# Optimization experiments

Hardware: AMD Instinct MI355X
Metric: run time of the kernel (lower is better)

Reference implementation:

```python
import jax, jax.numpy as jnp
import numpy as np

B, SEQ, D, H, E = 4, 4096, 1024, 4096, 8
CAPACITY = 2.0  # k = int(S * capacity) token-expert slots


def setup_inputs() -> dict:
    key = jax.random.key(0)
    ks = jax.random.split(key, 5)
    x = jax.random.normal(ks[0], (B, SEQ, D), dtype=jnp.float32)
    gate_weight = jax.random.normal(ks[1], (E, D), dtype=jnp.float32) * 0.006
    expert_bias = jnp.ones((E, 1), dtype=jnp.float32)
    W1 = jax.random.normal(ks[2], (E, D, H), dtype=jnp.float32) * 0.02
    b1 = jnp.zeros((E, H), dtype=jnp.float32)
    W2 = jax.random.normal(ks[3], (E, H, D), dtype=jnp.float32) * 0.02
    b2 = jnp.zeros((E, D), dtype=jnp.float32)
    return {"x": x, "gate_weight": gate_weight, "expert_bias": expert_bias,
            "W1": W1, "b1": b1, "W2": W2, "b2": b2}


def reference(x, gate_weight, expert_bias, W1, b1, W2, b2):
    Bv, s, Dv = x.shape
    xf = x.reshape(-1, Dv)               # [S, D]
    S = xf.shape[0]
    k = int(S * CAPACITY)

    # router: bias_sigmoid -> scores[e, s] = sigmoid(x @ gate.T + bias)
    logits = jnp.einsum('sd,ed->es', xf, gate_weight) + expert_bias  # [E, S]
    scores = jax.nn.sigmoid(logits)

    # global top-k over flattened (E*S) token-expert pairs
    value, index = jax.lax.top_k(scores.reshape(-1), k)
    index_expert = index // S
    index_token = index % S

    # combine weights: gating score at selected slots, 0 elsewhere (topk indices unique)
    C = jnp.zeros((E * S,), dtype=scores.dtype).at[index].set(value).reshape(E, S)

    token_each_expert = jax.ops.segment_sum(
        jnp.ones((k,), dtype=jnp.float32), index_expert, num_segments=E) / float(k)

    # per-expert MLP, gated combine (tokens with C==0 contribute exactly 0,
    # matching the torch gather/MLP/index_add_ path)
    out = jnp.zeros_like(xf)
    for e in range(E):
        h = jax.nn.gelu(xf @ W1[e] + b1[e], approximate=True)  # [S, H]
        y = h @ W2[e] + b2[e]                                  # [S, D]
        out = out + C[e][:, None] * y

    x_out = out.reshape(Bv, s, Dv)
    return x_out, token_each_expert, jnp.ones((E,), dtype=scores.dtype)
```

## Files before the change

### kernel.cpp

```cpp
#include <hip/hip_runtime.h>
#include <hip/hip_bf16.h>
#include <cstdint>
#include <cstdio>
#include <math.h>

#define S_TOK 16384
#define E_EXP 8
#define DDIM  1024
#define HDIM  4096
#define K_SEL 32768
#define ES    131072
#define OUT_XO 16777216

#define WS_META    0x000000u
#define WS_HIST    0x000100u
#define WS_COUNTS  0x001100u
#define WS_EXOFF   0x001200u
#define WS_TIEIDX  0x001300u
#define WS_CLEAR   0x00A000u
#define WS_TOK     0x010000u
#define WS_COEF    0x090000u
#define WS_SCORES  0x110000u
#define WS_TCNT    0x190000u
#define WS_TSLOT   0x1A0000u
#define WS_XB      0x400000u
#define WS_W1T    0x2400000u
#define WS_W2T    0x6400000u
#define WS_HBUF   0xA400000u
#define WS_TOTAL  0x1A400000u
#define WS_YBUF   WS_W1T

typedef __attribute__((ext_vector_type(4))) float f32x4;
typedef __attribute__((ext_vector_type(8))) short bf16x8;

__device__ __forceinline__ void gload_lds16(const void* g, void* l) {
  __builtin_amdgcn_global_load_lds((const __attribute__((address_space(1))) void*)g,
                                   (__attribute__((address_space(3))) void*)l, 16, 0, 0);
}

__device__ __forceinline__ float gelu_f(float x) {
  float u = __builtin_fmaf(x * x * x, 0.044715f, x);
  float e = __builtin_amdgcn_exp2f(-2.302207976f * u);
  return x * __builtin_amdgcn_rcpf(1.0f + e);
}

#define ABUF0 0
#define ABUF1 32768
#define BBUF0 65536
#define BBUF1 98304
#define HALF  16384

#define PH_BAR() __builtin_amdgcn_s_barrier()
#define VMC0M()  asm volatile("s_waitcnt vmcnt(0)" ::: "memory")

#define STAGE_A(DST, KE) do { \
  gload_lds16(aS00 + (KE), lds + (DST) + w * 2048); \
  gload_lds16(aS01 + (KE), lds + (DST) + w * 2048 + 1024); \
  gload_lds16(aS10 + (KE), lds + (DST) + HALF + w * 2048); \
  gload_lds16(aS11 + (KE), lds + (DST) + HALF + w * 2048 + 1024); } while (0)
#define STAGE_B(DST, KE) do { \
  gload_lds16(bS00 + (KE), lds + (DST) + w * 2048); \
  gload_lds16(bS01 + (KE), lds + (DST) + w * 2048 + 1024); \
  gload_lds16(bS10 + (KE), lds + (DST) + HALF + w * 2048); \
  gload_lds16(bS11 + (KE), lds + (DST) + HALF + w * 2048 + 1024); } while (0)

#define LDS_A03(AB) { _Pragma("unroll") for (int ii = 0; ii < 4; ii++) { \
  a03[ii][0] = *(const bf16x8*)(lds + (AB) + arow + ii * 2048 + pc0); \
  a03[ii][1] = *(const bf16x8*)(lds + (AB) + arow + ii * 2048 + pc1); } }
#define LDS_A47(AB) { _Pragma("unroll") for (int ii = 0; ii < 4; ii++) { \
  a47[ii][0] = *(const bf16x8*)(lds + (AB) + arow + (4 + ii) * 2048 + pc0); \
  a47[ii][1] = *(const bf16x8*)(lds + (AB) + arow + (4 + ii) * 2048 + pc1); } }
#define LDS_B01(BB) { _Pragma("unroll") for (int jj = 0; jj < 2; jj++) { \
  b01[jj][0] = *(const bf16x8*)(lds + (BB) + brow + jj * 2048 + pc0); \
  b01[jj][1] = *(const bf16x8*)(lds + (BB) + brow + jj * 2048 + pc1); } }
#define LDS_B23(BB) { _Pragma("unroll") for (int jj = 0; jj < 2; jj++) { \
  b23[jj][0] = *(const bf16x8*)(lds + (BB) + brow + (2 + jj) * 2048 + pc0); \
  b23[jj][1] = *(const bf16x8*)(lds + (BB) + brow + (2 + jj) * 2048 + pc1); } }

#define MF(AA, BF, IL, JL) { _Pragma("unroll") for (int ii = 0; ii < 4; ii++) \
  _Pragma("unroll") for (int jj = 0; jj < 2; jj++) { \
    acc[(IL)+ii][(JL)+jj] = __builtin_amdgcn_mfma_f32_16x16x32_bf16(AA[ii][0], BF[jj][0], acc[(IL)+ii][(JL)+jj], 0, 0, 0); \
    acc[(IL)+ii][(JL)+jj] = __builtin_amdgcn_mfma_f32_16x16x32_bf16(AA[ii][1], BF[jj][1], acc[(IL)+ii][(JL)+jj], 0, 0, 0); } }

#define TILE(T, AB, BB, ABn, BBn, STGA, STGB) do { \
  PH_BAR(); \
  LDS_A03(AB); \
  if (STGA) STAGE_A(ABn, ((T) + 1) * 64); \
  __builtin_amdgcn_s_setprio(1); MF(a03, b01, 0, 0); MF(a03, b23, 0, 2); __builtin_amdgcn_s_setprio(0); \
  VMC0M(); \
  PH_BAR(); \
  LDS_A47(AB); \
  if (STGB) STAGE_B(BB, ((T) + 2) * 64); \
  __builtin_amdgcn_s_setprio(1); MF(a47, b01, 4, 0); __builtin_amdgcn_s_setprio(0); \
  LDS_B01(BBn); \
  __builtin_amdgcn_s_setprio(1); MF(a47, b23, 4, 2); __builtin_amdgcn_s_setprio(0); \
  LDS_B23(BBn); \
} while (0)

#define TILE_LAST(AB, BB) do { \
  PH_BAR(); \
  LDS_A03(AB); \
  __builtin_amdgcn_s_setprio(1); MF(a03, b01, 0, 0); MF(a03, b23, 0, 2); __builtin_amdgcn_s_setprio(0); \
  PH_BAR(); \
  LDS_A47(AB); \
  __builtin_amdgcn_s_setprio(1); MF(a47, b01, 4, 0); MF(a47, b23, 4, 2); __builtin_amdgcn_s_setprio(0); \
} while (0)

__global__ __launch_bounds__(256) void transpose_bf16_kernel(
    const float* __restrict__ in, __hip_bfloat16* __restrict__ outp, int R, int C)
{
  __shared__ float tile[32][33];
  const int c0 = blockIdx.x * 32, r0 = blockIdx.y * 32;
  const size_t eoff = (size_t)blockIdx.z * (size_t)R * (size_t)C;
  const float* ip = in + eoff;
  __hip_bfloat16* op = outp + eoff;
  const int tx = threadIdx.x, ty = threadIdx.y;
#pragma unroll
  for (int i = 0; i < 4; i++) {
    int r = ty + i * 8;
    tile[r][tx] = ip[(size_t)(r0 + r) * C + c0 + tx];
  }
  __syncthreads();
#pragma unroll
  for (int i = 0; i < 4; i++) {
    int c = ty + i * 8;
    op[(size_t)(c0 + c) * R + r0 + tx] = __float2bfloat16(tile[tx][c]);
  }
}

__global__ __launch_bounds__(256) void router_kernel(
    const float* __restrict__ x, const float* __restrict__ gw, const float* __restrict__ bias,
    float* __restrict__ scores, __hip_bfloat16* __restrict__ xb)
{
  __shared__ float g[E_EXP * DDIM];
  __shared__ float bs[E_EXP];
  const int tid = threadIdx.x;
  for (int i = tid; i < E_EXP * DDIM; i += 256) g[i] = gw[i];
  if (tid < E_EXP) bs[tid] = bias[tid];
  __syncthreads();
  const int w = tid >> 6, lane = tid & 63;
  const int s = blockIdx.x * 4 + w;
  double acc[E_EXP] = {0, 0, 0, 0, 0, 0, 0, 0};
  const float* xrow = x + (size_t)s * DDIM;
  __hip_bfloat16* xbrow = xb + (size_t)s * DDIM;
#pragma unroll 4
  for (int j = 0; j < 16; j++) {
    int d = lane + 64 * j;
    float xv = xrow[d];
    xbrow[d] = __float2bfloat16(xv);
#pragma unroll
    for (int e = 0; e < E_EXP; e++) acc[e] += (double)xv * (double)g[e * DDIM + d];
  }
#pragma unroll
  for (int e = 0; e < E_EXP; e++) {
    double a = acc[e];
#pragma unroll
    for (int off = 32; off > 0; off >>= 1) a += __shfl_xor(a, off);
    acc[e] = a;
  }
  if (lane == 0) {
#pragma unroll
    for (int e = 0; e < E_EXP; e++) {
      double lg = acc[e] + (double)bs[e];
      float sc = (float)(1.0 / (1.0 + exp(-lg)));
      scores[(size_t)e * S_TOK + s] = sc;
    }
  }
}

__global__ __launch_bounds__(256) void hist_pass_kernel(
    const float* __restrict__ scores, const unsigned* __restrict__ meta,
    unsigned* __restrict__ hist, int pass)
{
  __shared__ unsigned h[256];
  const int tid = threadIdx.x;
  h[tid] = 0;
  __syncthreads();
  const unsigned prefix = meta[0];
  const int pshift = 32 - 8 * pass;
  const int bshift = 24 - 8 * pass;
  const unsigned base = blockIdx.x * 2048 + tid;
#pragma unroll
  for (int i = 0; i < 8; i++) {
    unsigned b = __float_as_uint(scores[base + i * 256]);
    bool ok = (pass == 0) || ((b >> pshift) == prefix);
    if (ok) atomicAdd(&h[(b >> bshift) & 0xFFu], 1u);
  }
  __syncthreads();
  if (h[tid]) atomicAdd(&hist[tid], h[tid]);
}

__global__ __launch_bounds__(256) void scan_pass_kernel(
    const unsigned* __restrict__ hist, unsigned* __restrict__ meta, int final)
{
  const int t = threadIdx.x;
  const unsigned v = hist[t];
  const unsigned prefix = meta[0];
  const unsigned above = meta[1];
  __shared__ unsigned csum[256];
  csum[t] = v;
  __syncthreads();
  for (int off = 1; off < 256; off <<= 1) {
    unsigned add = (t + off < 256) ? csum[t + off] : 0u;
    __syncthreads();
    csum[t] += add;
    __syncthreads();
  }
  const unsigned cge = csum[t];
  const unsigned cgt = cge - v;
  if (above + cgt < K_SEL && above + cge >= K_SEL) {
    meta[0] = (prefix << 8) | (unsigned)t;
    meta[1] = above + cgt;
    if (final) {
      meta[2] = (prefix << 8) | (unsigned)t;
      meta[4] = K_SEL - (above + cgt);
    }
  }
}

__global__ __launch_bounds__(256) void sel_kernel(const float* __restrict__ scores,
                                                  unsigned* __restrict__ meta,
                                                  unsigned* __restrict__ counts,
                                                  int* __restrict__ tok_list,
                                                  float* __restrict__ coef_list,
                                                  unsigned* __restrict__ tie_idx,
                                                  unsigned* __restrict__ tcnt,
                                                  unsigned* __restrict__ tslot)
{
  __shared__ unsigned lcnt[E_EXP], lbase[E_EXP];
  const int tid = threadIdx.x;
  if (tid < E_EXP) lcnt[tid] = 0;
  __syncthreads();
  const unsigned i = blockIdx.x * 256 + tid;
  const float v = scores[i];
  const unsigned b = __float_as_uint(v);
  const unsigned t = meta[2];
  const bool sel = (b > t);
  const unsigned e = i >> 14;
  unsigned myslot = 0;
  if (sel) myslot = atomicAdd(&lcnt[e], 1u);
  else if (b == t) {
    unsigned ts = atomicAdd(&meta[5], 1u);
    if (ts < 8192u) tie_idx[ts] = i;
  }
  __syncthreads();
  if (tid < E_EXP) lbase[tid] = atomicAdd(&counts[tid], lcnt[tid]);
  __syncthreads();
  if (sel) {
    const unsigned slot = lbase[e] + myslot;
    const unsigned p = e * S_TOK + slot;
    const unsigned tok = i & 16383u;
    tok_list[p] = (int)tok;
    coef_list[p] = v;
    unsigned us = atomicAdd(&tcnt[tok], 1u);
    tslot[tok * 8u + us] = (e << 14) | slot;
  }
}

__global__ __launch_bounds__(256) void fin_kernel(const unsigned* __restrict__ meta,
                                                  const unsigned* __restrict__ tie_idx,
                                                  unsigned* __restrict__ counts,
                                                  int* __restrict__ tok_list,
                                                  float* __restrict__ coef_list,
                                                  unsigned* __restrict__ tcnt,
                                                  unsigned* __restrict__ tslot)
{
  unsigned tcnt_ties = meta[5]; if (tcnt_ties > 8192u) tcnt_ties = 8192u;
  const unsigned q = meta[4];
  const float tval = __uint_as_float(meta[2]);
  for (unsigned t = threadIdx.x; t < tcnt_ties; t += 256) {
    unsigned idx = tie_idx[t];
    unsigned rank = 0;
    for (unsigned u = 0; u < tcnt_ties; u++) rank += (tie_idx[u] < idx) ? 1u : 0u;
    if (rank < q) {
      const unsigned e = idx >> 14;
      const unsigned tok = idx & 16383u;
      const unsigned slot = atomicAdd(&counts[e], 1u);
      tok_list[e * S_TOK + slot] = (int)tok;
      coef_list[e * S_TOK + slot] = tval;
      unsigned us = atomicAdd(&tcnt[tok], 1u);
      tslot[tok * 8u + us] = (e << 14) | slot;
    }
  }
}

__global__ void tail_kernel(const unsigned* __restrict__ counts, unsigned* __restrict__ exoff,
                            float* __restrict__ tail)
{
  if (threadIdx.x == 0) {
    unsigned o = 0;
    for (int e = 0; e < E_EXP; e++) { exoff[e] = o; o += counts[e]; }
    exoff[E_EXP] = o;
  }
  if (threadIdx.x < E_EXP) {
    tail[threadIdx.x] = (float)counts[threadIdx.x] * (1.0f / (float)K_SEL);
    tail[E_EXP + threadIdx.x] = 1.0f;
  }
}

__global__ __launch_bounds__(512, 1) void gemm1_kernel(
    const __hip_bfloat16* __restrict__ xb,
    const __hip_bfloat16* __restrict__ w1t,
    const float* __restrict__ b1,
    const int* __restrict__ tok_list,
    const unsigned* __restrict__ counts,
    const unsigned* __restrict__ exoff,
    __hip_bfloat16* __restrict__ hbuf)
{
  const int e = blockIdx.z;
  const int cnt = (int)counts[e];
  const int m0 = blockIdx.y * 256;
  if (m0 >= cnt) return;
  const int n0 = blockIdx.x * 256;

  __shared__ __align__(16) char lds[131072];
  __shared__ int s_tok[256];

  const int tid = threadIdx.x;
  const int w = tid >> 6, lane = tid & 63;
  const int wm = w >> 2, wn = w & 3;

  if (tid < 256) {
    int mi = m0 + tid;
    s_tok[tid] = tok_list[e * S_TOK + (mi < cnt ? mi : cnt - 1)];
  }
  __syncthreads();

  const int srl0 = w * 16 + (lane >> 3);
  const int srl1 = srl0 + 8;
  const int gch = ((lane & 7) ^ (lane >> 3)) * 8;
  const __hip_bfloat16* aS00 = xb + (size_t)s_tok[srl0] * DDIM + gch;
  const __hip_bfloat16* aS01 = xb + (size_t)s_tok[srl1] * DDIM + gch;
  const __hip_bfloat16* aS10 = xb + (size_t)s_tok[128 + srl0] * DDIM + gch;
  const __hip_bfloat16* aS11 = xb + (size_t)s_tok[128 + srl1] * DDIM + gch;
  const __hip_bfloat16* w1e = w1t + (size_t)e * HDIM * DDIM;
  const __hip_bfloat16* bS00 = w1e + (size_t)(n0 + srl0) * DDIM + gch;
  const __hip_bfloat16* bS01 = w1e + (size_t)(n0 + srl1) * DDIM + gch;
  const __hip_bfloat16* bS10 = w1e + (size_t)(n0 + 128 + srl0) * DDIM + gch;
  const __hip_bfloat16* bS11 = w1e + (size_t)(n0 + 128 + srl1) * DDIM + gch;

  const int arow = (wm * 128 + (lane & 15)) * 128;
  const int brow = (wn * 64 + (lane & 15)) * 128;
  const int pc0 = (((lane >> 4)) ^ (lane & 7)) * 16;
  const int pc1 = (((lane >> 4) + 4) ^ (lane & 7)) * 16;

  f32x4 acc[8][4] = {};
  bf16x8 a03[4][2], a47[4][2], b01[2][2], b23[2][2];

  STAGE_A(ABUF0, 0);
  STAGE_B(BBUF0, 0);
  STAGE_B(BBUF1, 64);
  VMC0M();
  PH_BAR();
  LDS_B01(BBUF0); LDS_B23(BBUF0);

  const int NKT = DDIM / 64;
  int kt = 0;
  for (; kt + 2 < NKT; kt += 2) {
    TILE(kt,     ABUF0, BBUF0, ABUF1, BBUF1, true, true);
    TILE(kt + 1, ABUF1, BBUF1, ABUF0, BBUF0, true, true);
  }
  TILE(kt, ABUF0, BBUF0, ABUF1, BBUF1, true, false);
  TILE_LAST(ABUF1, BBUF1);
  __syncthreads();

  __hip_bfloat16* stg = (__hip_bfloat16*)lds;
  const float* b1e = b1 + (size_t)e * HDIM;
  float bvj[4];
#pragma unroll
  for (int j = 0; j < 4; j++) bvj[j] = b1e[n0 + wn * 64 + j * 16 + (lane & 15)];
  const int pbase = (int)exoff[e] + m0;

#pragma unroll
  for (int P = 0; P < 4; P++) {
    __syncthreads();
    if (wm == (P >> 1)) {
      const int ib = (P & 1) * 4;
#pragma unroll
      for (int ii = 0; ii < 4; ii++)
#pragma unroll
        for (int jj = 0; jj < 4; jj++)
#pragma unroll
          for (int r = 0; r < 4; r++) {
            const int rloc = ii * 16 + (lane >> 4) * 4 + r;
            const int col = wn * 64 + jj * 16 + (lane & 15);
            stg[rloc * 264 + col] = __float2bfloat16(gelu_f(acc[ib + ii][jj][r] + bvj[jj]));
          }
    }
    __syncthreads();
    const int rr = tid >> 3;
    const int m = P * 64 + rr;
    if (m0 + m < cnt) {
      __hip_bfloat16* dst = hbuf + (size_t)(pbase + m) * HDIM + n0;
      const __hip_bfloat16* src = stg + rr * 264;
#pragma unroll
      for (int c = 0; c < 4; c++)
        *(uint4*)(dst + (tid & 7) * 8 + c * 64) = *(const uint4*)(src + (tid & 7) * 8 + c * 64);
    }
  }
}

__global__ __launch_bounds__(512, 1) void gemm2_kernel(
    const __hip_bfloat16* __restrict__ hbuf,
    const __hip_bfloat16* __restrict__ w2t,
    const float* __restrict__ b2,
    const float* __restrict__ coef_list,
    const unsigned* __restrict__ counts,
    const unsigned* __restrict__ exoff,
    __hip_bfloat16* __restrict__ ybuf)
{
  const int e = blockIdx.z;
  const int cnt = (int)counts[e];
  const int m0 = blockIdx.y * 256;
  if (m0 >= cnt) return;
  const int n0 = blockIdx.x * 256;

  __shared__ __align__(16) char lds[131072];
  __shared__ float s_coef[256];

  const int tid = threadIdx.x;
  const int w = tid >> 6, lane = tid & 63;
  const int wm = w >> 2, wn = w & 3;
  const int pb = (int)exoff[e];

  if (tid < 256) {
    int mi = m0 + tid;
    s_coef[tid] = (mi < cnt) ? coef_list[e * S_TOK + mi] : 0.0f;
  }
  __syncthreads();

  const int srl0 = w * 16 + (lane >> 3);
  const int srl1 = srl0 + 8;
  const int gch = ((lane & 7) ^ (lane >> 3)) * 8;
  const int ra0 = pb + ((m0 + srl0 < cnt) ? m0 + srl0 : cnt - 1);
  const int ra1 = pb + ((m0 + srl1 < cnt) ? m0 + srl1 : cnt - 1);
  const int ra2 = pb + ((m0 + 128 + srl0 < cnt) ? m0 + 128 + srl0 : cnt - 1);
  const int ra3 = pb + ((m0 + 128 + srl1 < cnt) ? m0 + 128 + srl1 : cnt - 1);
  const __hip_bfloat16* aS00 = hbuf + (size_t)ra0 * HDIM + gch;
  const __hip_bfloat16* aS01 = hbuf + (size_t)ra1 * HDIM + gch;
  const __hip_bfloat16* aS10 = hbuf + (size_t)ra2 * HDIM + gch;
  const __hip_bfloat16* aS11 = hbuf + (size_t)ra3 * HDIM + gch;
  const __hip_bfloat16* w2e = w2t + (size_t)e * DDIM * HDIM;
  const __hip_bfloat16* bS00 = w2e + (size_t)(n0 + srl0) * HDIM + gch;
  const __hip_bfloat16* bS01 = w2e + (size_t)(n0 + srl1) * HDIM + gch;
  const __hip_bfloat16* bS10 = w2e + (size_t)(n0 + 128 + srl0) * HDIM + gch;
  const __hip_bfloat16* bS11 = w2e + (size_t)(n0 + 128 + srl1) * HDIM + gch;

  const int arow = (wm * 128 + (lane & 15)) * 128;
  const int brow = (wn * 64 + (lane & 15)) * 128;
  const int pc0 = (((lane >> 4)) ^ (lane & 7)) * 16;
  const int pc1 = (((lane >> 4) + 4) ^ (lane & 7)) * 16;

  f32x4 acc[8][4] = {};
  bf16x8 a03[4][2], a47[4][2], b01[2][2], b23[2][2];

  STAGE_A(ABUF0, 0);
  STAGE_B(BBUF0, 0);
  STAGE_B(BBUF1, 64);
  VMC0M();
  PH_BAR();
  LDS_B01(BBUF0); LDS_B23(BBUF0);

  const int NKT = HDIM / 64;
  int kt = 0;
  for (; kt + 2 < NKT; kt += 2) {
    TILE(kt,     ABUF0, BBUF0, ABUF1, BBUF1, true, true);
    TILE(kt + 1, ABUF1, BBUF1, ABUF0, BBUF0, true, true);
  }
  TILE(kt, ABUF0, BBUF0, ABUF1, BBUF1, true, false);
  TILE_LAST(ABUF1, BBUF1);
  __syncthreads();

  __hip_bfloat16* stg = (__hip_bfloat16*)lds;
  const float* b2e = b2 + (size_t)e * DDIM;
  float bvj[4];
#pragma unroll
  for (int j = 0; j < 4; j++) bvj[j] = b2e[n0 + wn * 64 + j * 16 + (lane & 15)];
  const int pbase = pb + m0;

#pragma unroll
  for (int P = 0; P < 4; P++) {
    __syncthreads();
    if (wm == (P >> 1)) {
      const int ib = (P & 1) * 4;
#pragma unroll
      for (int ii = 0; ii < 4; ii++)
#pragma unroll
        for (int jj = 0; jj < 4; jj++)
#pragma unroll
          for (int r = 0; r < 4; r++) {
            const int rloc = ii * 16 + (lane >> 4) * 4 + r;
            const int col = wn * 64 + jj * 16 + (lane & 15);
            const float cf = s_coef[P * 64 + rloc];
            stg[rloc * 264 + col] = __float2bfloat16(cf * (acc[ib + ii][jj][r] + bvj[jj]));
          }
    }
    __syncthreads();
    const int rr = tid >> 3;
    const int m = P * 64 + rr;
    if (m0 + m < cnt) {
      __hip_bfloat16* dst = ybuf + (size_t)(pbase + m) * DDIM + n0;
      const __hip_bfloat16* src = stg + rr * 264;
#pragma unroll
      for (int c = 0; c < 4; c++)
        *(uint4*)(dst + (tid & 7) * 8 + c * 64) = *(const uint4*)(src + (tid & 7) * 8 + c * 64);
    }
  }
}

__global__ __launch_bounds__(256) void combine_kernel(
    const __hip_bfloat16* __restrict__ ybuf,
    const unsigned* __restrict__ tcnt,
    const unsigned* __restrict__ tslot,
    const unsigned* __restrict__ exoff,
    float* __restrict__ out)
{
  const int tid = threadIdx.x;
  const int t = blockIdx.x * 2 + (tid >> 7);
  const int d0 = (tid & 127) * 8;
  float a[8] = {0, 0, 0, 0, 0, 0, 0, 0};
  const unsigned n = tcnt[t];
  for (unsigned s = 0; s < n; s++) {
    const unsigned code = tslot[t * 8u + s];
    const unsigned p = exoff[code >> 14] + (code & 16383u);
    bf16x8 v = *(const bf16x8*)(ybuf + (size_t)p * DDIM + d0);
#pragma unroll
    for (int k = 0; k < 8; k++)
      a[k] += __uint_as_float(((unsigned)(unsigned short)v[k]) << 16);
  }
  float* op = out + (size_t)t * DDIM + d0;
  *(float4*)op = make_float4(a[0], a[1], a[2], a[3]);
  *(float4*)(op + 4) = make_float4(a[4], a[5], a[6], a[7]);
}

extern "C" void kernel_launch(void* const* d_in, const int* in_sizes, int n_in,
                              void* d_out, int out_size, void* d_ws, size_t ws_size,
                              hipStream_t stream) {
  const float* x    = (const float*)d_in[0];
  const float* gw   = (const float*)d_in[1];
  const float* bias = (const float*)d_in[2];
  const float* W1   = (const float*)d_in[3];
  const float* b1   = (const float*)d_in[4];
  const float* W2   = (const float*)d_in[5];
  const float* b2   = (const float*)d_in[6];
  float* out = (float*)d_out;
  char* ws = (char*)d_ws;

  if (ws_size < (size_t)WS_TOTAL) {
    fprintf(stderr, "kernel_launch: ws_size %zu < required %u\n", ws_size, WS_TOTAL);
    return;
  }

  unsigned* meta   = (unsigned*)(ws + WS_META);
  unsigned* hist   = (unsigned*)(ws + WS_HIST);
  unsigned* counts = (unsigned*)(ws + WS_COUNTS);
  unsigned* exoff  = (unsigned*)(ws + WS_EXOFF);
  unsigned* tiei   = (unsigned*)(ws + WS_TIEIDX);
  unsigned* tcnt   = (unsigned*)(ws + WS_TCNT);
  unsigned* tslot  = (unsigned*)(ws + WS_TSLOT);
  int*      tokl   = (int*)(ws + WS_TOK);
  float*    coefl  = (float*)(ws + WS_COEF);
  float*    scores = (float*)(ws + WS_SCORES);
  __hip_bfloat16* xb   = (__hip_bfloat16*)(ws + WS_XB);
  __hip_bfloat16* w1t  = (__hip_bfloat16*)(ws + WS_W1T);
  __hip_bfloat16* w2t  = (__hip_bfloat16*)(ws + WS_W2T);
  __hip_bfloat16* hbuf = (__hip_bfloat16*)(ws + WS_HBUF);
  __hip_bfloat16* ybuf = (__hip_bfloat16*)(ws + WS_YBUF);

  hipMemsetAsync(ws, 0, WS_CLEAR, stream);
  hipMemsetAsync(ws + WS_TCNT, 0, S_TOK * sizeof(unsigned), stream);

  transpose_bf16_kernel<<<dim3(HDIM / 32, DDIM / 32, E_EXP), dim3(32, 8), 0, stream>>>(W1, w1t, DDIM, HDIM);
  transpose_bf16_kernel<<<dim3(DDIM / 32, HDIM / 32, E_EXP), dim3(32, 8), 0, stream>>>(W2, w2t, HDIM, DDIM);

  router_kernel<<<S_TOK / 4, 256, 0, stream>>>(x, gw, bias, scores, xb);

  for (int p = 0; p < 4; p++) {
    hist_pass_kernel<<<ES / 2048, 256, 0, stream>>>(scores, meta, hist + p * 256, p);
    scan_pass_kernel<<<1, 256, 0, stream>>>(hist + p * 256, meta, p == 3);
  }
  sel_kernel<<<ES / 256, 256, 0, stream>>>(scores, meta, counts, tokl, coefl, tiei, tcnt, tslot);
  fin_kernel<<<1, 256, 0, stream>>>(meta, tiei, counts, tokl, coefl, tcnt, tslot);
  tail_kernel<<<1, 64, 0, stream>>>(counts, exoff, out + OUT_XO);

  gemm1_kernel<<<dim3(HDIM / 256, S_TOK / 256, E_EXP), 512, 0, stream>>>(
      xb, w1t, b1, tokl, counts, exoff, hbuf);
  gemm2_kernel<<<dim3(DDIM / 256, S_TOK / 256, E_EXP), 512, 0, stream>>>(
      hbuf, w2t, b2, coefl, counts, exoff, ybuf);
  combine_kernel<<<S_TOK / 2, 256, 0, stream>>>(ybuf, tcnt, tslot, exoff, out);
}
```

Before: 947.0 us.

## Use partial vmcnt waits in GEMM pipeline and remap blocks across XCDs per expert

Replaces the full vmcnt(0) wait in each tile with partial waits placed just before the LDS reads that need the data. Global-to-LDS loads for the next tiles can then stay in flight while MFMAs run. It also flattens the 3D grid into a 1D grid and remaps block ids so consecutive ids, which are dealt round-robin across the 8 XCDs, place each expert's blocks on one XCD for better L2 reuse of that expert's weights. The risk is a wrong wait count causing a data race. The mapping also assumes 8 XCDs and can unbalance load when expert token counts differ.

```diff
diff --git a/kernel.cpp b/kernel.cpp
--- a/kernel.cpp
+++ b/kernel.cpp
@@ -52,6 +52,7 @@
 
 #define PH_BAR() __builtin_amdgcn_s_barrier()
 #define VMC0M()  asm volatile("s_waitcnt vmcnt(0)" ::: "memory")
+#define VMCN(N)  asm volatile("s_waitcnt vmcnt(" #N ")" ::: "memory")
 
 #define STAGE_A(DST, KE) do { \
   gload_lds16(aS00 + (KE), lds + (DST) + w * 2048); \
@@ -82,19 +83,20 @@
     acc[(IL)+ii][(JL)+jj] = __builtin_amdgcn_mfma_f32_16x16x32_bf16(AA[ii][0], BF[jj][0], acc[(IL)+ii][(JL)+jj], 0, 0, 0); \
     acc[(IL)+ii][(JL)+jj] = __builtin_amdgcn_mfma_f32_16x16x32_bf16(AA[ii][1], BF[jj][1], acc[(IL)+ii][(JL)+jj], 0, 0, 0); } }
 
-#define TILE(T, AB, BB, ABn, BBn, STGA, STGB) do { \
+#define TILE(T, AB, BB, ABn, BBn, STGA, STGB, NB, NA) do { \
   PH_BAR(); \
   LDS_A03(AB); \
   if (STGA) STAGE_A(ABn, ((T) + 1) * 64); \
   __builtin_amdgcn_s_setprio(1); MF(a03, b01, 0, 0); MF(a03, b23, 0, 2); __builtin_amdgcn_s_setprio(0); \
-  VMC0M(); \
   PH_BAR(); \
   LDS_A47(AB); \
   if (STGB) STAGE_B(BB, ((T) + 2) * 64); \
   __builtin_amdgcn_s_setprio(1); MF(a47, b01, 4, 0); __builtin_amdgcn_s_setprio(0); \
+  VMCN(NB); \
   LDS_B01(BBn); \
   __builtin_amdgcn_s_setprio(1); MF(a47, b23, 4, 2); __builtin_amdgcn_s_setprio(0); \
   LDS_B23(BBn); \
+  VMCN(NA); \
 } while (0)
 
 #define TILE_LAST(AB, BB) do { \
@@ -307,11 +309,14 @@
     const unsigned* __restrict__ exoff,
     __hip_bfloat16* __restrict__ hbuf)
 {
-  const int e = blockIdx.z;
+  const int id = blockIdx.x;
+  const int L = (id & 7) * 1024 + (id >> 3);
+  const int e = L >> 10;
+  const int rem = L & 1023;
   const int cnt = (int)counts[e];
-  const int m0 = blockIdx.y * 256;
+  const int m0 = (rem >> 4) * 256;
   if (m0 >= cnt) return;
-  const int n0 = blockIdx.x * 256;
+  const int n0 = (rem & 15) * 256;
 
   __shared__ __align__(16) char lds[131072];
   __shared__ int s_tok[256];
@@ -357,10 +362,10 @@
   const int NKT = DDIM / 64;
   int kt = 0;
   for (; kt + 2 < NKT; kt += 2) {
-    TILE(kt,     ABUF0, BBUF0, ABUF1, BBUF1, true, true);
-    TILE(kt + 1, ABUF1, BBUF1, ABUF0, BBUF0, true, true);
-  }
-  TILE(kt, ABUF0, BBUF0, ABUF1, BBUF1, true, false);
+    TILE(kt,     ABUF0, BBUF0, ABUF1, BBUF1, true, true, 8, 4);
+    TILE(kt + 1, ABUF1, BBUF1, ABUF0, BBUF0, true, true, 8, 4);
+  }
+  TILE(kt, ABUF0, BBUF0, ABUF1, BBUF1, true, false, 4, 0);
   TILE_LAST(ABUF1, BBUF1);
   __syncthreads();
 
@@ -409,11 +414,14 @@
     const unsigned* __restrict__ exoff,
     __hip_bfloat16* __restrict__ ybuf)
 {
-  const int e = blockIdx.z;
+  const int id = blockIdx.x;
+  const int L = (id & 7) * 256 + (id >> 3);
+  const int e = L >> 8;
+  const int rem = L & 255;
   const int cnt = (int)counts[e];
-  const int m0 = blockIdx.y * 256;
+  const int m0 = (rem >> 2) * 256;
   if (m0 >= cnt) return;
-  const int n0 = blockIdx.x * 256;
+  const int n0 = (rem & 3) * 256;
 
   __shared__ __align__(16) char lds[131072];
   __shared__ float s_coef[256];
@@ -464,10 +472,10 @@
   const int NKT = HDIM / 64;
   int kt = 0;
   for (; kt + 2 < NKT; kt += 2) {
-    TILE(kt,     ABUF0, BBUF0, ABUF1, BBUF1, true, true);
-    TILE(kt + 1, ABUF1, BBUF1, ABUF0, BBUF0, true, true);
-  }
-  TILE(kt, ABUF0, BBUF0, ABUF1, BBUF1, true, false);
+    TILE(kt,     ABUF0, BBUF0, ABUF1, BBUF1, true, true, 8, 4);
+    TILE(kt + 1, ABUF1, BBUF1, ABUF0, BBUF0, true, true, 8, 4);
+  }
+  TILE(kt, ABUF0, BBUF0, ABUF1, BBUF1, true, false, 4, 0);
   TILE_LAST(ABUF1, BBUF1);
   __syncthreads();
 
@@ -583,9 +591,7 @@
   fin_kernel<<<1, 256, 0, stream>>>(meta, tiei, counts, tokl, coefl, tcnt, tslot);
   tail_kernel<<<1, 64, 0, stream>>>(counts, exoff, out + OUT_XO);
 
-  gemm1_kernel<<<dim3(HDIM / 256, S_TOK / 256, E_EXP), 512, 0, stream>>>(
-      xb, w1t, b1, tokl, counts, exoff, hbuf);
-  gemm2_kernel<<<dim3(DDIM / 256, S_TOK / 256, E_EXP), 512, 0, stream>>>(
-      hbuf, w2t, b2, coefl, counts, exoff, ybuf);
+  gemm1_kernel<<<8192, 512, 0, stream>>>(xb, w1t, b1, tokl, counts, exoff, hbuf);
+  gemm2_kernel<<<2048, 512, 0, stream>>>(hbuf, w2t, b2, coefl, counts, exoff, ybuf);
   combine_kernel<<<S_TOK / 2, 256, 0, stream>>>(ybuf, tcnt, tslot, exoff, out);
 }
```

Measured after the change: 860.1 us. 1.1x faster.
